# Optimization experiments

Hardware: AMD Instinct MI355X
Metric: run time of the kernel (lower is better)

The kernel has to match this reference:

```python
import jax, jax.numpy as jnp
import numpy as np

EPS = 1e-12  # torch f.normalize eps


def _rms_norm(x, g):
    # f.normalize(x, dim=1) * g * sqrt(C): L2-normalize over channel dim
    c = x.shape[1]
    n = jnp.maximum(jnp.linalg.norm(x, axis=1, keepdims=True), EPS)
    return x / n * g * (c ** 0.5)


def setup_inputs() -> dict:
    key = jax.random.key(0)
    ks = jax.random.split(key, 5)
    b, dim, H, W = 32, 256, 64, 64
    heads, dim_head, num_mem = 4, 32, 4
    hidden = heads * dim_head
    return {
        "x": jax.random.normal(ks[0], (b, dim, H, W), dtype=jnp.float32),
        "g1": jnp.ones((1, dim, 1, 1), dtype=jnp.float32),
        "mem_kv": jax.random.normal(ks[1], (2, heads, dim_head, num_mem), dtype=jnp.float32),
        "w_qkv": jax.random.normal(ks[2], (3 * hidden, dim), dtype=jnp.float32) * (1.0 / np.sqrt(dim)),
        "w_out": jax.random.normal(ks[3], (dim, hidden), dtype=jnp.float32) * (1.0 / np.sqrt(hidden)),
        "b_out": jnp.zeros((dim,), dtype=jnp.float32),
        "g2": jnp.ones((1, dim, 1, 1), dtype=jnp.float32),
    }


def reference(x, g1, mem_kv, w_qkv, w_out, b_out, g2):
    b, c, H, W = x.shape
    _, heads, dim_head, num_mem = mem_kv.shape
    n = H * W
    scale = dim_head ** -0.5

    xn = _rms_norm(x, g1)
    # 1x1 conv qkv projection: [b, 3*hidden, H, W]
    qkv = jnp.einsum('oc,bchw->bohw', w_qkv, xn)
    hidden = heads * dim_head
    q, k, v = jnp.split(qkv, 3, axis=1)
    # b (h d) x y -> b h d (x y)
    q = q.reshape(b, heads, dim_head, n)
    k = k.reshape(b, heads, dim_head, n)
    v = v.reshape(b, heads, dim_head, n)

    mk = jnp.broadcast_to(mem_kv[0], (b, heads, dim_head, num_mem))
    mv = jnp.broadcast_to(mem_kv[1], (b, heads, dim_head, num_mem))
    k = jnp.concatenate([mk, k], axis=-1)
    v = jnp.concatenate([mv, v], axis=-1)

    q = jax.nn.softmax(q, axis=-2) * scale  # softmax over head dim d
    k = jax.nn.softmax(k, axis=-1)          # softmax over sequence n

    context = jnp.einsum('bhdn,bhen->bhde', k, v)   # [b,h,d,e]
    out = jnp.einsum('bhde,bhdn->bhen', context, q)  # [b,h,e,n]
    out = out.reshape(b, hidden, H, W)

    o = jnp.einsum('oc,bchw->bohw', w_out, out) + b_out[None, :, None, None]
    return _rms_norm(o, g2)
```

## Files before the change

kernel.cpp:

```cpp
#include <hip/hip_runtime.h>
#include <math.h>

#define CC   256
#define HW   4096
#define OC3  384
#define HID  128
#define DH   32
#define NM   4
#define NPART 8
#define SCALE 0.17677669529663688f

typedef __bf16 bf16x8 __attribute__((ext_vector_type(8)));
typedef float  f32x4  __attribute__((ext_vector_type(4)));

__device__ __forceinline__ ushort f2bf(float x) {
    union { float f; unsigned u; } v; v.f = x;
    unsigned r = v.u + 0x7fffu + ((v.u >> 16) & 1u);
    return (ushort)(r >> 16);
}
__device__ __forceinline__ float bf2f(ushort b) {
    union { unsigned u; float f; } v; v.u = ((unsigned)b) << 16; return v.f;
}
__device__ __forceinline__ void g2l16(const void* g, void* l) {
    __builtin_amdgcn_global_load_lds(
        (const __attribute__((address_space(1))) void*)g,
        (__attribute__((address_space(3))) void*)l, 16, 0, 0);
}

__global__ void k_prep(const float* __restrict__ wqkv, const float* __restrict__ g1,
                       const float* __restrict__ wout,
                       ushort* __restrict__ wq2t, ushort* __restrict__ woutt) {
    int o = blockIdx.x, t = threadIdx.x;
    wq2t[(size_t)o * CC + t] = f2bf(wqkv[(size_t)o * CC + t] * g1[t] * 16.0f);
    if (o < CC && t < HID) woutt[(size_t)o * HID + t] = f2bf(wout[(size_t)o * HID + t]);
}

__global__ __launch_bounds__(256) void k_qkv(const ushort* __restrict__ wq2t,
        const float* __restrict__ x, ushort* __restrict__ qkv) {
    __shared__ __align__(16) ushort As[128 * 32];
    __shared__ __align__(16) ushort Bs[128 * 40];
    __shared__ __align__(16) float  xt[32 * 132];
    __shared__ float nrm[256];
    __shared__ float invp[128];
    int tid = threadIdx.x;
    int lin = blockIdx.x + 3 * (blockIdx.y + 32 * blockIdx.z);
    int swz = (lin & 7) * 384 + (lin >> 3);
    int m0 = (swz % 3) * 128;
    int t_ = swz / 3;
    int p0 = (t_ & 31) * 128;
    int b  = t_ >> 5;
    int lane = tid & 63, wid = tid >> 6;
    int l15 = tid & 15, quad = (tid >> 4) & 3;
    int wm = wid >> 1, wn = wid & 1;
    int rsub = lane >> 2, csub = (lane & 3) * 8;
    int cb = tid >> 5;
    int p4 = (tid & 31) * 4;
    int tpix = tid & 127;
    int tc8  = (tid >> 7) * 8;
    const ushort* Ab = wq2t + (size_t)m0 * CC;
    const float*  xb = x + ((size_t)b * CC) * HW + p0;
    float psum = 0.f;
    f32x4 acc[4][4];
    #pragma unroll
    for (int i = 0; i < 4; ++i)
        #pragma unroll
        for (int j = 0; j < 4; ++j) acc[i][j] = (f32x4){0.f, 0.f, 0.f, 0.f};
    for (int k0 = 0; k0 < CC; k0 += 32) {
        __syncthreads();
        #pragma unroll
        for (int q = 0; q < 2; ++q) {
            int rw = wid * 32 + q * 16;
            g2l16(Ab + (size_t)(rw + rsub) * CC + k0 + csub, &As[rw * 32]);
        }
        #pragma unroll
        for (int rr = 0; rr < 4; ++rr) {
            int c = rr * 8 + cb;
            float4 v = *(const float4*)&xb[(size_t)(k0 + c) * HW + p4];
            *(float4*)&xt[c * 132 + p4] = v;
        }
        __syncthreads();
        #pragma unroll
        for (int rr = 0; rr < 2; ++rr) {
            int c8 = tc8 + rr * 16;
            uint4 pk; ushort* o8 = (ushort*)&pk;
            #pragma unroll
            for (int i = 0; i < 8; ++i) {
                float v = xt[(c8 + i) * 132 + tpix];
                psum += v * v;
                o8[i] = f2bf(v);
            }
            *(uint4*)&Bs[tpix * 40 + c8] = pk;
        }
        __syncthreads();
        bf16x8 af[4], bfr[4];
        #pragma unroll
        for (int mt = 0; mt < 4; ++mt)
            af[mt] = *(const bf16x8*)&As[(wm * 64 + mt * 16 + l15) * 32 + quad * 8];
        #pragma unroll
        for (int nt = 0; nt < 4; ++nt)
            bfr[nt] = *(const bf16x8*)&Bs[(wn * 64 + nt * 16 + l15) * 40 + quad * 8];
        #pragma unroll
        for (int mt = 0; mt < 4; ++mt)
            #pragma unroll
            for (int nt = 0; nt < 4; ++nt)
                acc[mt][nt] = __builtin_amdgcn_mfma_f32_16x16x32_bf16(
                                  af[mt], bfr[nt], acc[mt][nt], 0, 0, 0);
    }
    nrm[tid] = psum;
    __syncthreads();
    if (tid < 128) {
        float s = nrm[tid] + nrm[tid + 128];
        invp[tid] = 1.0f / fmaxf(sqrtf(s), 1e-12f);
    }
    __syncthreads();
    #pragma unroll
    for (int mt = 0; mt < 4; ++mt) {
        int o = m0 + wm * 64 + mt * 16 + quad * 4;
        #pragma unroll
        for (int nt = 0; nt < 4; ++nt) {
            int pixl = wn * 64 + nt * 16 + l15;
            float iv = invp[pixl];
            ushort* dst = qkv + ((size_t)(b * OC3 + o)) * HW + p0 + pixl;
            #pragma unroll
            for (int r = 0; r < 4; ++r) dst[(size_t)r * HW] = f2bf(acc[mt][nt][r] * iv);
        }
    }
}

__global__ void k_ksoft(const ushort* __restrict__ qkv, const float* __restrict__ memkv,
                        float* __restrict__ kmaxb, float* __restrict__ rsumb) {
    int row = blockIdx.x * 4 + (threadIdx.x >> 6);
    int lane = threadIdx.x & 63;
    int b = row >> 7, hd = row & 127;
    const ushort* kp = qkv + ((size_t)(b * OC3 + HID + hd)) * HW;
    float m = -1e30f;
    #pragma unroll
    for (int i0 = 0; i0 < HW; i0 += 512) {
        uint4 pk = *(const uint4*)&kp[i0 + lane * 8];
        const ushort* e = (const ushort*)&pk;
        #pragma unroll
        for (int j = 0; j < 8; ++j) m = fmaxf(m, bf2f(e[j]));
    }
    #pragma unroll
    for (int s = 1; s < 64; s <<= 1) m = fmaxf(m, __shfl_xor(m, s));
    const float* mk = memkv + hd * NM;
    #pragma unroll
    for (int j = 0; j < NM; ++j) m = fmaxf(m, mk[j]);
    float s = 0.f;
    #pragma unroll
    for (int i0 = 0; i0 < HW; i0 += 512) {
        uint4 pk = *(const uint4*)&kp[i0 + lane * 8];
        const ushort* e = (const ushort*)&pk;
        #pragma unroll
        for (int j = 0; j < 8; ++j) s += __expf(bf2f(e[j]) - m);
    }
    #pragma unroll
    for (int t = 1; t < 64; t <<= 1) s += __shfl_xor(s, t);
    #pragma unroll
    for (int j = 0; j < NM; ++j) s += __expf(mk[j] - m);
    if (lane == 0) { kmaxb[row] = m; rsumb[row] = 1.0f / s; }
}

__global__ __launch_bounds__(256) void k_ctx(const ushort* __restrict__ qkv,
        const float* __restrict__ memkv, const float* __restrict__ kmaxb,
        const float* __restrict__ rsumb, float* __restrict__ ctxp) {
    __shared__ float kl[DH][65];
    __shared__ float vl[DH][65];
    __shared__ float red[256 * 33];
    int tid = threadIdx.x;
    int bh = blockIdx.x;
    int part = blockIdx.y;
    int b = bh >> 2, h = bh & 3;
    int lr = tid >> 3;
    int nn8 = (tid & 7) * 8;
    const ushort* kp = qkv + ((size_t)(b * OC3 + HID + h * DH) + lr) * HW + part * 512 + nn8;
    const ushort* vp = qkv + ((size_t)(b * OC3 + 2 * HID + h * DH) + lr) * HW + part * 512 + nn8;
    int rowbase = bh * DH;
    float kmr = kmaxb[rowbase + lr], rsr = rsumb[rowbase + lr];
    int slot = tid & 31, nng = tid >> 5;
    int d0 = (slot >> 2) * 4, e0 = (slot & 3) * 8;
    float acc[4][8];
    #pragma unroll
    for (int i = 0; i < 4; ++i)
        #pragma unroll
        for (int j = 0; j < 8; ++j) acc[i][j] = 0.f;
    for (int n0 = 0; n0 < 512; n0 += 64) {
        __syncthreads();
        uint4 kv4 = *(const uint4*)&kp[n0];
        uint4 vv4 = *(const uint4*)&vp[n0];
        const ushort* ke = (const ushort*)&kv4;
        const ushort* ve = (const ushort*)&vv4;
        #pragma unroll
        for (int j = 0; j < 8; ++j) {
            kl[lr][nn8 + j] = __expf(bf2f(ke[j]) - kmr) * rsr;
            vl[lr][nn8 + j] = bf2f(ve[j]);
        }
        __syncthreads();
        #pragma unroll 2
        for (int t = 0; t < 8; ++t) {
            int nn = nng * 8 + t;
            float kv[4], vv[8];
            #pragma unroll
            for (int i = 0; i < 4; ++i) kv[i] = kl[d0 + i][nn];
            #pragma unroll
            for (int j = 0; j < 8; ++j) vv[j] = vl[e0 + j][nn];
            #pragma unroll
            for (int i = 0; i < 4; ++i)
                #pragma unroll
                for (int j = 0; j < 8; ++j) acc[i][j] += kv[i] * vv[j];
        }
    }
    __syncthreads();
    #pragma unroll
    for (int i = 0; i < 4; ++i)
        #pragma unroll
        for (int j = 0; j < 8; ++j) red[tid * 33 + i * 8 + j] = acc[i][j];
    __syncthreads();
    #pragma unroll
    for (int q = 0; q < 4; ++q) {
        int o = tid * 4 + q;
        int d = o >> 5, e = o & 31;
        int sl = (d >> 2) * 4 + (e >> 3);
        int k = (d & 3) * 8 + (e & 7);
        float s = 0.f;
        #pragma unroll
        for (int g = 0; g < 8; ++g) s += red[(g * 32 + sl) * 33 + k];
        if (part == 0) {
            float km = kmaxb[rowbase + d], rsm = rsumb[rowbase + d];
            #pragma unroll
            for (int m = 0; m < NM; ++m) {
                float kw = __expf(memkv[(h * DH + d) * NM + m] - km) * rsm;
                s += kw * memkv[512 + (h * DH + e) * NM + m];
            }
        }
        ctxp[(size_t)part * 131072 + (size_t)bh * 1024 + o] = s;
    }
}

__global__ __launch_bounds__(256) void k_w2(const float* __restrict__ ctxp,
        const ushort* __restrict__ woutt, ushort* __restrict__ W2) {
    __shared__ ushort ctxb[4 * 32 * 40];
    int tid = threadIdx.x, b = blockIdx.x;
    int wid = tid >> 6;
    int l15 = tid & 15, quad = (tid >> 4) & 3;
    #pragma unroll
    for (int j = 0; j < 16; ++j) {
        int idx = tid + j * 256;
        float s = 0.f;
        #pragma unroll
        for (int p = 0; p < NPART; ++p)
            s += ctxp[(size_t)p * 131072 + (size_t)b * 4096 + idx];
        int h = idx >> 10, d = (idx >> 5) & 31, e = idx & 31;
        ctxb[(h * 32 + d) * 40 + e] = f2bf(s);
    }
    __syncthreads();
    #pragma unroll
    for (int h = 0; h < 4; ++h) {
        f32x4 acc[4][2];
        #pragma unroll
        for (int i = 0; i < 4; ++i)
            #pragma unroll
            for (int j = 0; j < 2; ++j) acc[i][j] = (f32x4){0.f, 0.f, 0.f, 0.f};
        bf16x8 af[4], bfr[2];
        #pragma unroll
        for (int mt = 0; mt < 4; ++mt)
            af[mt] = *(const bf16x8*)&woutt[(size_t)(wid * 64 + mt * 16 + l15) * HID
                                            + h * DH + quad * 8];
        #pragma unroll
        for (int nt = 0; nt < 2; ++nt)
            bfr[nt] = *(const bf16x8*)&ctxb[(h * 32 + nt * 16 + l15) * 40 + quad * 8];
        #pragma unroll
        for (int mt = 0; mt < 4; ++mt)
            #pragma unroll
            for (int nt = 0; nt < 2; ++nt)
                acc[mt][nt] = __builtin_amdgcn_mfma_f32_16x16x32_bf16(
                                  af[mt], bfr[nt], acc[mt][nt], 0, 0, 0);
        #pragma unroll
        for (int mt = 0; mt < 4; ++mt)
            #pragma unroll
            for (int nt = 0; nt < 2; ++nt)
                #pragma unroll
                for (int r = 0; r < 4; ++r) {
                    int oc = wid * 64 + mt * 16 + quad * 4 + r;
                    int d  = nt * 16 + l15;
                    W2[((size_t)b * CC + oc) * HID + h * DH + d] = f2bf(acc[mt][nt][r]);
                }
    }
}

__global__ __launch_bounds__(256) void k_final(const ushort* __restrict__ qkv,
        const ushort* __restrict__ W2, const float* __restrict__ bout,
        const float* __restrict__ g2, float* __restrict__ y) {
    __shared__ __align__(16) ushort sq[64 * 136];
    __shared__ __align__(16) ushort Ws[256 * 32];
    __shared__ float red[64 * 17];
    __shared__ float invs[64];
    __shared__ float bl[256];
    __shared__ float gl[256];
    int tid = threadIdx.x;
    int b = blockIdx.y;
    int hwb = blockIdx.x * 64;
    int lane = tid & 63, wid = tid >> 6;
    int l15 = tid & 15, quad = (tid >> 4) & 3;
    bl[tid] = bout[tid];
    gl[tid] = g2[tid];

    {
        const ushort* qp = qkv + ((size_t)b * OC3 + wid * DH) * HW + hwb + lane;
        float vd[32];
        float m = -1e30f;
        #pragma unroll
        for (int d = 0; d < 32; ++d) {
            float v = bf2f(qp[(size_t)d * HW]);
            vd[d] = v; m = fmaxf(m, v);
        }
        float s = 0.f;
        #pragma unroll
        for (int d = 0; d < 32; ++d) { float e = __expf(vd[d] - m); vd[d] = e; s += e; }
        float r_ = SCALE / s;
        #pragma unroll
        for (int q8 = 0; q8 < 4; ++q8) {
            uint4 pk; ushort* o8 = (ushort*)&pk;
            #pragma unroll
            for (int i = 0; i < 8; ++i) o8[i] = f2bf(vd[q8 * 8 + i] * r_);
            *(uint4*)&sq[lane * 136 + wid * DH + q8 * 8] = pk;
        }
    }

    f32x4 acc[4][4];
    #pragma unroll
    for (int i = 0; i < 4; ++i)
        #pragma unroll
        for (int j = 0; j < 4; ++j) acc[i][j] = (f32x4){0.f, 0.f, 0.f, 0.f};
    int rsub = lane >> 2, csub = (lane & 3) * 8;
    const ushort* W2b = W2 + (size_t)b * CC * HID;
    for (int k0 = 0; k0 < HID; k0 += 32) {
        __syncthreads();
        #pragma unroll
        for (int q = 0; q < 4; ++q) {
            int rw = wid * 64 + q * 16;
            g2l16(W2b + (size_t)(rw + rsub) * HID + k0 + csub, &Ws[rw * 32]);
        }
        __syncthreads();
        bf16x8 af[4], bfr[4];
        #pragma unroll
        for (int mt = 0; mt < 4; ++mt)
            af[mt] = *(const bf16x8*)&Ws[(wid * 64 + mt * 16 + l15) * 32 + quad * 8];
        #pragma unroll
        for (int nt = 0; nt < 4; ++nt)
            bfr[nt] = *(const bf16x8*)&sq[(nt * 16 + l15) * 136 + k0 + quad * 8];
        #pragma unroll
        for (int mt = 0; mt < 4; ++mt)
            #pragma unroll
            for (int nt = 0; nt < 4; ++nt)
                acc[mt][nt] = __builtin_amdgcn_mfma_f32_16x16x32_bf16(
                                  af[mt], bfr[nt], acc[mt][nt], 0, 0, 0);
    }

    float part[4] = {0.f, 0.f, 0.f, 0.f};
    #pragma unroll
    for (int mt = 0; mt < 4; ++mt)
        #pragma unroll
        for (int r = 0; r < 4; ++r) {
            int oc = wid * 64 + mt * 16 + quad * 4 + r;
            float bo = bl[oc];
            #pragma unroll
            for (int nt = 0; nt < 4; ++nt) {
                float v = acc[mt][nt][r] + bo;
                acc[mt][nt][r] = v;
                part[nt] += v * v;
            }
        }
    __syncthreads();
    #pragma unroll
    for (int nt = 0; nt < 4; ++nt)
        red[(nt * 16 + l15) * 17 + wid * 4 + quad] = part[nt];
    __syncthreads();
    if (tid < 64) {
        float s = 0.f;
        #pragma unroll
        for (int g = 0; g < 16; ++g) s += red[tid * 17 + g];
        invs[tid] = 1.0f / fmaxf(sqrtf(s), 1e-12f);
    }
    __syncthreads();
    #pragma unroll
    for (int mt = 0; mt < 4; ++mt)
        #pragma unroll
        for (int nt = 0; nt < 4; ++nt) {
            int pix = nt * 16 + l15;
            float iv = invs[pix];
            #pragma unroll
            for (int r = 0; r < 4; ++r) {
                int oc = wid * 64 + mt * 16 + quad * 4 + r;
                y[((size_t)(b * CC + oc)) * HW + hwb + pix] = acc[mt][nt][r] * iv * gl[oc] * 16.0f;
            }
        }
}

extern "C" void kernel_launch(void* const* d_in, const int* in_sizes, int n_in,
                              void* d_out, int out_size, void* d_ws, size_t ws_size,
                              hipStream_t stream) {
    const float* x     = (const float*)d_in[0];
    const float* g1    = (const float*)d_in[1];
    const float* memkv = (const float*)d_in[2];
    const float* wqkv  = (const float*)d_in[3];
    const float* wout  = (const float*)d_in[4];
    const float* bout  = (const float*)d_in[5];
    const float* g2    = (const float*)d_in[6];
    float* y = (float*)d_out;

    char* w = (char*)d_ws;
    ushort* wq2t  = (ushort*)w;  w += (size_t)OC3 * CC * 2;
    ushort* woutt = (ushort*)w;  w += (size_t)CC * HID * 2;
    float*  kmaxb = (float*)w;   w += 4096 * 4;
    float*  rsumb = (float*)w;   w += 4096 * 4;
    float*  ctxp  = (float*)w;   w += (size_t)NPART * 131072 * 4;
    ushort* W2    = (ushort*)w;  w += (size_t)32 * CC * HID * 2;
    ushort* qkv   = (ushort*)w;  w += (size_t)32 * OC3 * HW * 2;

    k_prep  <<<dim3(384),       dim3(256), 0, stream>>>(wqkv, g1, wout, wq2t, woutt);
    k_qkv   <<<dim3(3, 32, 32), dim3(256), 0, stream>>>(wq2t, x, qkv);
    k_ksoft <<<dim3(1024),      dim3(256), 0, stream>>>(qkv, memkv, kmaxb, rsumb);
    k_ctx   <<<dim3(128, 8),    dim3(256), 0, stream>>>(qkv, memkv, kmaxb, rsumb, ctxp);
    k_w2    <<<dim3(32),        dim3(256), 0, stream>>>(ctxp, woutt, W2);
    k_final <<<dim3(64, 32),    dim3(256), 0, stream>>>(qkv, W2, bout, g2, y);
}
```

Before: 358.2 us.

## Double-buffer qkv GEMM tiles and load x directly into bf16 B tile

The qkv projection kernel now double-buffers the A and B shared-memory tiles, staging the next K slice while MFMAs run on the current one, which cuts three barriers per iteration down to one. The fp32 transpose staging buffer is removed: each thread reads its pixel's channels straight from global memory, accumulates the squared norm and packs bf16 into the B tile. Each per-thread global read is now a scalar load strided by HW rather than a float4, though consecutive threads still touch consecutive pixels, so accesses stay coalesced. LDS use is roughly unchanged.

```diff
diff --git a/kernel.cpp b/kernel.cpp
--- a/kernel.cpp
+++ b/kernel.cpp
@@ -37,9 +37,8 @@
 
 __global__ __launch_bounds__(256) void k_qkv(const ushort* __restrict__ wq2t,
         const float* __restrict__ x, ushort* __restrict__ qkv) {
-    __shared__ __align__(16) ushort As[128 * 32];
-    __shared__ __align__(16) ushort Bs[128 * 40];
-    __shared__ __align__(16) float  xt[32 * 132];
+    __shared__ __align__(16) ushort As[2][128 * 32];
+    __shared__ __align__(16) ushort Bs[2][128 * 40];
     __shared__ float nrm[256];
     __shared__ float invp[128];
     int tid = threadIdx.x;
@@ -53,58 +52,57 @@
     int l15 = tid & 15, quad = (tid >> 4) & 3;
     int wm = wid >> 1, wn = wid & 1;
     int rsub = lane >> 2, csub = (lane & 3) * 8;
-    int cb = tid >> 5;
-    int p4 = (tid & 31) * 4;
     int tpix = tid & 127;
     int tc8  = (tid >> 7) * 8;
     const ushort* Ab = wq2t + (size_t)m0 * CC;
-    const float*  xb = x + ((size_t)b * CC) * HW + p0;
+    const float*  xg = x + ((size_t)b * CC) * HW + p0 + tpix;
     float psum = 0.f;
     f32x4 acc[4][4];
     #pragma unroll
     for (int i = 0; i < 4; ++i)
         #pragma unroll
         for (int j = 0; j < 4; ++j) acc[i][j] = (f32x4){0.f, 0.f, 0.f, 0.f};
-    for (int k0 = 0; k0 < CC; k0 += 32) {
-        __syncthreads();
+
+    auto stage = [&](int buf, int k0) {
+        float xv[16];
+        #pragma unroll
+        for (int i = 0; i < 8; ++i) xv[i]     = xg[(size_t)(k0 + tc8 + i) * HW];
+        #pragma unroll
+        for (int i = 0; i < 8; ++i) xv[8 + i] = xg[(size_t)(k0 + tc8 + 16 + i) * HW];
+        uint4 pka, pkb; ushort* oa = (ushort*)&pka; ushort* ob = (ushort*)&pkb;
+        #pragma unroll
+        for (int i = 0; i < 8; ++i) { float v = xv[i];     psum += v * v; oa[i] = f2bf(v); }
+        #pragma unroll
+        for (int i = 0; i < 8; ++i) { float v = xv[8 + i]; psum += v * v; ob[i] = f2bf(v); }
+        *(uint4*)&Bs[buf][tpix * 40 + tc8]      = pka;
+        *(uint4*)&Bs[buf][tpix * 40 + tc8 + 16] = pkb;
         #pragma unroll
         for (int q = 0; q < 2; ++q) {
             int rw = wid * 32 + q * 16;
-            g2l16(Ab + (size_t)(rw + rsub) * CC + k0 + csub, &As[rw * 32]);
-        }
-        #pragma unroll
-        for (int rr = 0; rr < 4; ++rr) {
-            int c = rr * 8 + cb;
-            float4 v = *(const float4*)&xb[(size_t)(k0 + c) * HW + p4];
-            *(float4*)&xt[c * 132 + p4] = v;
-        }
-        __syncthreads();
-        #pragma unroll
-        for (int rr = 0; rr < 2; ++rr) {
-            int c8 = tc8 + rr * 16;
-            uint4 pk; ushort* o8 = (ushort*)&pk;
-            #pragma unroll
-            for (int i = 0; i < 8; ++i) {
-                float v = xt[(c8 + i) * 132 + tpix];
-                psum += v * v;
-                o8[i] = f2bf(v);
-            }
-            *(uint4*)&Bs[tpix * 40 + c8] = pk;
-        }
-        __syncthreads();
+            g2l16(Ab + (size_t)(rw + rsub) * CC + k0 + csub, &As[buf][rw * 32]);
+        }
+    };
+
+    stage(0, 0);
+    __syncthreads();
+    #pragma unroll
+    for (int s = 0; s < 8; ++s) {
+        int cur = s & 1;
         bf16x8 af[4], bfr[4];
         #pragma unroll
         for (int mt = 0; mt < 4; ++mt)
-            af[mt] = *(const bf16x8*)&As[(wm * 64 + mt * 16 + l15) * 32 + quad * 8];
+            af[mt] = *(const bf16x8*)&As[cur][(wm * 64 + mt * 16 + l15) * 32 + quad * 8];
         #pragma unroll
         for (int nt = 0; nt < 4; ++nt)
-            bfr[nt] = *(const bf16x8*)&Bs[(wn * 64 + nt * 16 + l15) * 40 + quad * 8];
+            bfr[nt] = *(const bf16x8*)&Bs[cur][(wn * 64 + nt * 16 + l15) * 40 + quad * 8];
         #pragma unroll
         for (int mt = 0; mt < 4; ++mt)
             #pragma unroll
             for (int nt = 0; nt < 4; ++nt)
                 acc[mt][nt] = __builtin_amdgcn_mfma_f32_16x16x32_bf16(
                                   af[mt], bfr[nt], acc[mt][nt], 0, 0, 0);
+        if (s < 7) stage(cur ^ 1, (s + 1) * 32);
+        __syncthreads();
     }
     nrm[tid] = psum;
     __syncthreads();
```

Result: slower. 422.4 us (+17.9%).
